# Performance work log

Hardware: AMD Instinct MI355X
Metric: run time of the kernel (lower is better)

The kernel has to match this reference:

```python
import jax, jax.numpy as jnp
import numpy as np

B, S, D, H = 2, 2048, 1024, 16
DK = D // H


def setup_inputs() -> dict:
    key = jax.random.key(0)
    ks = jax.random.split(key, 12)
    scale = 0.02  # keep exp(QK^T) finite in fp32
    return {
        "query": jax.random.normal(ks[0], (B, S, D), jnp.float32),
        "key_": jax.random.normal(ks[1], (B, S, D), jnp.float32),
        "value": jax.random.normal(ks[2], (B, S, D), jnp.float32),
        "mask": jax.random.randint(ks[3], (B, S, S), 0, 2, jnp.int32),
        "Wq": scale * jax.random.normal(ks[4], (D, D), jnp.float32),
        "bq": jnp.zeros((D,), jnp.float32),
        "Wk": scale * jax.random.normal(ks[5], (D, D), jnp.float32),
        "bk": jnp.zeros((D,), jnp.float32),
        "Wv": scale * jax.random.normal(ks[6], (D, D), jnp.float32),
        "bv": jnp.zeros((D,), jnp.float32),
        "Wo": scale * jax.random.normal(ks[7], (D, D), jnp.float32),
        "bo": jnp.zeros((D,), jnp.float32),
    }


def reference(query, key_, value, mask, Wq, bq, Wk, bk, Wv, bv, Wo, bo):
    b, s, d = query.shape
    # torch Linear: x @ W.T + b, then split heads -> [b, h, s, d_k]
    def proj(x, W, bias):
        return (x @ W.T + bias).reshape(b, s, H, DK).transpose(0, 2, 1, 3)

    q = proj(query, Wq, bq)
    k = proj(key_, Wk, bk)
    v = proj(value, Wv, bv)

    # non-standard: exp(QK^T) / sqrt(d_k), then mask, then softmax
    scores = jnp.exp(jnp.einsum("bhqd,bhkd->bhqk", q, k)) / jnp.sqrt(
        jnp.asarray(DK, q.dtype)
    )
    scores = jnp.where(mask[:, None, :, :] == 0, jnp.asarray(-1e9, q.dtype), scores)
    p_attn = jax.nn.softmax(scores, axis=-1)

    out = jnp.einsum("bhqk,bhkd->bhqd", p_attn, v)  # [b, h, s, d_k]
    out = out.transpose(0, 2, 1, 3).reshape(b, s, d)  # merge heads
    return out @ Wo.T + bo
```

## Files before the change

kernel.cpp:

```cpp
#include <hip/hip_runtime.h>
#include <math.h>

#define B_ 2
#define S_ 2048
#define D_ 1024
#define H_ 16
#define DK_ 64
#define M_ (B_*S_)

typedef __attribute__((ext_vector_type(8))) _Float16 f16x8;
typedef __attribute__((ext_vector_type(4))) _Float16 f16x4;
typedef __attribute__((ext_vector_type(2))) __fp16 fp16x2;
typedef __attribute__((ext_vector_type(4))) float f32x4;

#define MFMA16(a,b,c) __builtin_amdgcn_mfma_f32_16x16x32_f16((a),(b),(c),0,0,0)

__device__ __forceinline__ void gload16(const void* g, void* l) {
    __builtin_amdgcn_global_load_lds(
        (const __attribute__((address_space(1))) unsigned int*)g,
        (__attribute__((address_space(3))) unsigned int*)l, 16, 0, 0);
}

__global__ __launch_bounds__(256)
void splitmask(const float* __restrict__ query, const float* __restrict__ key_,
               const float* __restrict__ value,
               const float* __restrict__ Wq, const float* __restrict__ Wk,
               const float* __restrict__ Wv, const float* __restrict__ Wo,
               const int* __restrict__ mask, unsigned long long* __restrict__ mbits,
               _Float16* __restrict__ Xhq, _Float16* __restrict__ Xlq,
               _Float16* __restrict__ Xhk, _Float16* __restrict__ Xlk,
               _Float16* __restrict__ Xhv,
               _Float16* __restrict__ hq, _Float16* __restrict__ lq,
               _Float16* __restrict__ hk, _Float16* __restrict__ lk,
               _Float16* __restrict__ hv, _Float16* __restrict__ ho)
{
    if (blockIdx.x >= 8192) {
        int wid  = (blockIdx.x - 8192) * 4 + (threadIdx.x >> 6);
        int lane = threadIdx.x & 63;
        int v = mask[(size_t)wid * 64 + lane];
        unsigned long long bal = __ballot(v != 0);
        if (lane == 0) mbits[wid] = bal;
        return;
    }
    int t = blockIdx.x * 256 + threadIdx.x;
    int region = t >> 19;
    int u = t & 524287;
    const float* src; _Float16* dhi; _Float16* dlo; size_t e;
    if (region < 3) {
        e = (size_t)u * 8;
        src = (region == 0) ? query : (region == 1) ? key_ : value;
        dhi = (region == 0) ? Xhq : (region == 1) ? Xhk : Xhv;
        dlo = (region == 0) ? Xlq : (region == 1) ? Xlk : nullptr;
    } else {
        int mi = u >> 17;
        e = (size_t)(u & 131071) * 8;
        src = (mi == 0) ? Wq : (mi == 1) ? Wk : (mi == 2) ? Wv : Wo;
        dhi = (mi == 0) ? hq : (mi == 1) ? hk : (mi == 2) ? hv : ho;
        dlo = (mi == 0) ? lq : (mi == 1) ? lk : nullptr;
    }
    float4 a = *(const float4*)&src[e];
    float4 b = *(const float4*)&src[e + 4];
    float v[8] = {a.x, a.y, a.z, a.w, b.x, b.y, b.z, b.w};
    f16x8 hi, lo;
    #pragma unroll
    for (int j = 0; j < 8; ++j) {
        float s = v[j] * 64.f;
        _Float16 h = (_Float16)s;
        hi[j] = h; lo[j] = (_Float16)(s - (float)h);
    }
    *(f16x8*)&dhi[e] = hi;
    if (dlo) *(f16x8*)&dlo[e] = lo;
}

template<int NPROD, int OUT_MODE>
__device__ __forceinline__
void gemm_body2(char* smem, const _Float16* __restrict__ Ah,
                const _Float16* __restrict__ Al,
                const _Float16* __restrict__ Bh, const _Float16* __restrict__ Bl,
                const float* __restrict__ bias, void* __restrict__ outp, int gid)
{
    constexpr int BUFSZ = (NPROD == 3) ? 32768 : 16384;
    const int tid  = threadIdx.x;
    const int lane = tid & 63, w = tid >> 6;
    const int lx   = lane & 15, lg = lane >> 4;
    const int wm   = w >> 1, wn = w & 1;

    int nid = (gid & 7) * 32 + (gid >> 3);
    const int colBase = (nid & 7) * 128;
    const int rowBase = (nid >> 3) * 128;

    const int sRow = (lane >> 2);
    const int sChk = (lane & 3) ^ ((lane >> 2) & 3);

    auto STAGE = [&](int buf, int k0) {
        char* base = smem + buf * BUFSZ;
        #pragma unroll
        for (int ii = 0; ii < 2; ++ii) {
            int i = w * 2 + ii;
            int r = i * 16 + sRow;
            gload16(Ah + (size_t)(rowBase + r) * D_ + k0 + sChk * 8, base + i * 1024);
            gload16(Bh + (size_t)(colBase + r) * D_ + k0 + sChk * 8, base + 8192 + i * 1024);
            if (NPROD == 3) {
                gload16(Al + (size_t)(rowBase + r) * D_ + k0 + sChk * 8, base + 16384 + i * 1024);
                gload16(Bl + (size_t)(colBase + r) * D_ + k0 + sChk * 8, base + 24576 + i * 1024);
            }
        }
    };

    f32x4 acc[4][4];
    #pragma unroll
    for (int i = 0; i < 4; ++i)
        #pragma unroll
        for (int j = 0; j < 4; ++j) acc[i][j] = (f32x4){0.f, 0.f, 0.f, 0.f};

    STAGE(0, 0);
    __syncthreads();
    int cur = 0;
    for (int k0 = 0; k0 < D_; k0 += 32) {
        if (k0 + 32 < D_) STAGE(cur ^ 1, k0 + 32);
        char* base = smem + cur * BUFSZ;
        _Float16* AhS = (_Float16*)base;
        _Float16* BhS = (_Float16*)(base + 8192);
        _Float16* AlS = (_Float16*)(base + 16384);
        _Float16* BlS = (_Float16*)(base + 24576);

        f16x8 bh[4], bl[4];
        #pragma unroll
        for (int fj = 0; fj < 4; ++fj) {
            int brow = wn * 64 + fj * 16 + lx;
            bh[fj] = *(const f16x8*)((char*)BhS + brow * 64 + 16 * (lg ^ (brow & 3)));
            if (NPROD == 3)
                bl[fj] = *(const f16x8*)((char*)BlS + brow * 64 + 16 * (lg ^ (brow & 3)));
        }
        #pragma unroll
        for (int fi = 0; fi < 4; ++fi) {
            int arow = wm * 64 + fi * 16 + lx;
            f16x8 ah = *(const f16x8*)((char*)AhS + arow * 64 + 16 * (lg ^ (arow & 3)));
            f16x8 al;
            if (NPROD == 3)
                al = *(const f16x8*)((char*)AlS + arow * 64 + 16 * (lg ^ (arow & 3)));
            #pragma unroll
            for (int fj = 0; fj < 4; ++fj) {
                acc[fi][fj] = MFMA16(ah, bh[fj], acc[fi][fj]);
                if (NPROD == 3) {
                    acc[fi][fj] = MFMA16(ah, bl[fj], acc[fi][fj]);
                    acc[fi][fj] = MFMA16(al, bh[fj], acc[fi][fj]);
                }
            }
        }
        __syncthreads();
        cur ^= 1;
    }

    constexpr float INV = 1.f / 4096.f;
    #pragma unroll
    for (int fi = 0; fi < 4; ++fi) {
        #pragma unroll
        for (int fj = 0; fj < 4; ++fj) {
            int n = colBase + wn * 64 + fj * 16 + lx;
            float bv = bias[n];
            if (OUT_MODE == 1) {
                _Float16* Ohi = (_Float16*)outp;
                _Float16* Olo = Ohi + (size_t)M_ * D_;
                int hh = n >> 6, d = n & 63;
                #pragma unroll
                for (int rr = 0; rr < 4; ++rr) {
                    int m = rowBase + wm * 64 + fi * 16 + lg * 4 + rr;
                    int bb = m >> 11, s = m & 2047;
                    float val = acc[fi][fj][rr] * INV + bv;
                    _Float16 hv = (_Float16)val;
                    size_t o = (((size_t)bb * H_ + hh) * S_ + s) * DK_ + d;
                    Ohi[o] = hv;
                    Olo[o] = (_Float16)(val - (float)hv);
                }
            } else {
                _Float16* Vt = (_Float16*)outp;
                int hh = n >> 6, d = n & 63;
                int m0 = rowBase + wm * 64 + fi * 16 + lg * 4;
                int bb = m0 >> 11, s = m0 & 2047;
                f16x4 pk;
                #pragma unroll
                for (int rr = 0; rr < 4; ++rr)
                    pk[rr] = (_Float16)(acc[fi][fj][rr] * INV + bv);
                *(f16x4*)&Vt[(((size_t)bb * H_ + hh) * DK_ + d) * S_ + s] = pk;
            }
        }
    }
}

__global__ __launch_bounds__(256)
void proj3(const _Float16* __restrict__ Xhq, const _Float16* __restrict__ Xlq,
           const _Float16* __restrict__ Xhk, const _Float16* __restrict__ Xlk,
           const _Float16* __restrict__ Xhv,
           const _Float16* __restrict__ WhiQ, const _Float16* __restrict__ WloQ,
           const _Float16* __restrict__ WhiK, const _Float16* __restrict__ WloK,
           const _Float16* __restrict__ WhiV,
           const float* __restrict__ bq, const float* __restrict__ bk,
           const float* __restrict__ bv,
           _Float16* __restrict__ Qhi, _Float16* __restrict__ Khi,
           _Float16* __restrict__ VtW)
{
    extern __shared__ char smem[];
    int mode = blockIdx.x >> 8;
    int gid  = blockIdx.x & 255;
    if (mode == 0)
        gemm_body2<3, 1>(smem, Xhq, Xlq, WhiQ, WloQ, bq, Qhi, gid);
    else if (mode == 1)
        gemm_body2<3, 1>(smem, Xhk, Xlk, WhiK, WloK, bk, Khi, gid);
    else
        gemm_body2<1, 2>(smem, Xhv, nullptr, WhiV, nullptr, bv, VtW, gid);
}

__global__ __launch_bounds__(256)
void gemm64(const _Float16* __restrict__ Ap, const _Float16* __restrict__ Bhi,
            const float* __restrict__ bias, float* __restrict__ out)
{
    __shared__ __attribute__((aligned(16))) char smem[24576];

    const int tid  = threadIdx.x;
    const int lane = tid & 63, w = tid >> 6;
    const int lx   = lane & 15, lg = lane >> 4;
    const int wm   = w >> 1, wn = w & 1;

    int gid = blockIdx.x;
    int nid = (gid & 7) * 64 + (gid >> 3);
    const int colBase = (nid & 7) * 128;
    const int rowBase = (nid >> 3) * 64;

    const int sRow = (lane >> 2);
    const int sChk = (lane & 3) ^ ((lane >> 2) & 3);

    auto STAGE = [&](int buf, int k0) {
        char* base = smem + buf * 12288;
        gload16(Ap + (size_t)(rowBase + w * 16 + sRow) * D_ + k0 + sChk * 8,
                base + w * 1024);
        #pragma unroll
        for (int ii = 0; ii < 2; ++ii) {
            int i = w * 2 + ii;
            int r = i * 16 + sRow;
            gload16(Bhi + (size_t)(colBase + r) * D_ + k0 + sChk * 8,
                    base + 4096 + i * 1024);
        }
    };

    f32x4 acc[2][4];
    #pragma unroll
    for (int i = 0; i < 2; ++i)
        #pragma unroll
        for (int j = 0; j < 4; ++j) acc[i][j] = (f32x4){0.f, 0.f, 0.f, 0.f};

    STAGE(0, 0);
    __syncthreads();
    int cur = 0;
    for (int k0 = 0; k0 < D_; k0 += 32) {
        if (k0 + 32 < D_) STAGE(cur ^ 1, k0 + 32);
        char* base = smem + cur * 12288;
        _Float16* AS = (_Float16*)base;
        _Float16* BS = (_Float16*)(base + 4096);

        f16x8 bh[4];
        #pragma unroll
        for (int fj = 0; fj < 4; ++fj) {
            int brow = wn * 64 + fj * 16 + lx;
            bh[fj] = *(const f16x8*)((char*)BS + brow * 64 + 16 * (lg ^ (brow & 3)));
        }
        #pragma unroll
        for (int fi = 0; fi < 2; ++fi) {
            int arow = wm * 32 + fi * 16 + lx;
            f16x8 ah = *(const f16x8*)((char*)AS + arow * 64 + 16 * (lg ^ (arow & 3)));
            #pragma unroll
            for (int fj = 0; fj < 4; ++fj)
                acc[fi][fj] = MFMA16(ah, bh[fj], acc[fi][fj]);
        }
        __syncthreads();
        cur ^= 1;
    }

    constexpr float INV = 1.f / 64.f;
    #pragma unroll
    for (int fi = 0; fi < 2; ++fi) {
        #pragma unroll
        for (int fj = 0; fj < 4; ++fj) {
            int n = colBase + wn * 64 + fj * 16 + lx;
            float bv = bias[n];
            #pragma unroll
            for (int rr = 0; rr < 4; ++rr) {
                int m = rowBase + wm * 32 + fi * 16 + lg * 4 + rr;
                out[(size_t)m * D_ + n] = acc[fi][fj][rr] * INV + bv;
            }
        }
    }
}

__global__ __launch_bounds__(512, 4)
void flash_mfma(const _Float16* __restrict__ Qhi, const _Float16* __restrict__ Qlo,
                const _Float16* __restrict__ Khi, const _Float16* __restrict__ Klo,
                const _Float16* __restrict__ Vt, const unsigned long long* __restrict__ Mb,
                _Float16* __restrict__ octx)
{
    __shared__ __attribute__((aligned(16))) _Float16 Kbuf[2][2][64 * 64];
    __shared__ __attribute__((aligned(16))) _Float16 Vbuf[2][64 * 64];
    __shared__ __attribute__((aligned(16))) _Float16 PwS[8][16 * 64];

    const int tid  = threadIdx.x;
    const int lane = tid & 63;
    const int w    = tid >> 6;
    const int lx   = lane & 15;
    const int lg   = lane >> 4;

    int bid = blockIdx.x;
    int swz = (bid & 7) * 64 + (bid >> 3);
    int qb = swz & 15;
    int h  = (swz >> 4) & 15;
    int b  = swz >> 8;

    const int q0 = qb * 128;
    const size_t bh = (size_t)b * H_ + h;
    const _Float16* KhiG = Khi + bh * S_ * DK_;
    const _Float16* KloG = Klo + bh * S_ * DK_;
    const _Float16* VtG  = Vt  + bh * DK_ * S_;

    const int qrow = q0 + w * 16 + lx;
    f16x8 qh[2], ql[2];
    {
        const _Float16* ph = Qhi + bh * S_ * DK_ + (size_t)qrow * DK_ + lg * 8;
        const _Float16* pl = Qlo + bh * S_ * DK_ + (size_t)qrow * DK_ + lg * 8;
        qh[0] = *(const f16x8*)ph;
        qh[1] = *(const f16x8*)(ph + 32);
        ql[0] = *(const f16x8*)pl;
        ql[1] = *(const f16x8*)(pl + 32);
    }

    const unsigned long long* mrow = Mb + ((size_t)b * S_ + qrow) * (S_ / 64);
    constexpr float LN8 = 2.0794415416798357f;

    auto STAGE = [&](int buf, int t) {
        int rr = w * 8 + (lane >> 3);
        int cc = (lane & 7) ^ (lane >> 3);
        gload16(KhiG + (size_t)(t * 64 + rr) * DK_ + cc * 8, &Kbuf[buf][0][w * 512]);
        gload16(KloG + (size_t)(t * 64 + rr) * DK_ + cc * 8, &Kbuf[buf][1][w * 512]);
        gload16(VtG + (size_t)rr * S_ + t * 64 + cc * 8, &Vbuf[buf][w * 512]);
    };

    f32x4 oacc[4];
    float m_run = -1e30f, l_lane = 0.f;
    #pragma unroll
    for (int dt = 0; dt < 4; ++dt) oacc[dt] = (f32x4){0.f, 0.f, 0.f, 0.f};

    char* Pw = (char*)&PwS[w][0];

    STAGE(0, 0);
    int cur = 0;
    for (int t = 0; t < 32; ++t) {
        __syncthreads();
        if (t < 31) STAGE(cur ^ 1, t + 1);
        unsigned long long mw = mrow[t];
        const char* KH = (const char*)&Kbuf[cur][0][0];
        const char* KL = (const char*)&Kbuf[cur][1][0];
        const char* VB = (const char*)&Vbuf[cur][0];
        cur ^= 1;

        float sv[16];
        __builtin_amdgcn_s_setprio(1);
        #pragma unroll
        for (int ct = 0; ct < 4; ++ct) {
            int row  = ct * 16 + lx;
            int sw   = (row & 7) << 4;
            int base = row * 128 + lg * 16;
            f16x8 kh0 = *(const f16x8*)(KH + ((base +  0) ^ sw));
            f16x8 kh1 = *(const f16x8*)(KH + ((base + 64) ^ sw));
            f16x8 kl0 = *(const f16x8*)(KL + ((base +  0) ^ sw));
            f16x8 kl1 = *(const f16x8*)(KL + ((base + 64) ^ sw));
            f32x4 s = (f32x4){0.f, 0.f, 0.f, 0.f};
            s = MFMA16(kh0, qh[0], s);
            s = MFMA16(kh1, qh[1], s);
            s = MFMA16(kl0, qh[0], s);
            s = MFMA16(kl1, qh[1], s);
            s = MFMA16(kh0, ql[0], s);
            s = MFMA16(kh1, ql[1], s);
            #pragma unroll
            for (int r = 0; r < 4; ++r)
                sv[ct * 4 + r] = ((mw >> (lg * 4 + ct * 16 + r)) & 1ull)
                                   ? s[r] : -1e30f;
        }
        __builtin_amdgcn_s_setprio(0);

        float mx = fmaxf(fmaxf(fmaxf(sv[0], sv[1]), fmaxf(sv[2], sv[3])),
                         fmaxf(fmaxf(sv[4], sv[5]), fmaxf(sv[6], sv[7])));
        mx = fmaxf(mx, fmaxf(fmaxf(fmaxf(sv[8], sv[9]), fmaxf(sv[10], sv[11])),
                             fmaxf(fmaxf(sv[12], sv[13]), fmaxf(sv[14], sv[15]))));
        mx = fmaxf(mx, __shfl_xor(mx, 16));
        mx = fmaxf(mx, __shfl_xor(mx, 32));
        float tvmax = __expf(mx - LN8);

        if (__any(tvmax > m_run)) {
            float mn = fmaxf(m_run, tvmax);
            float scl = __expf(m_run - mn);
            m_run = mn;
            l_lane *= scl;
            #pragma unroll
            for (int dt = 0; dt < 4; ++dt)
                #pragma unroll
                for (int r = 0; r < 4; ++r) oacc[dt][r] *= scl;
        }

        float cut = (m_run >= 26.f) ? __logf(m_run - 25.f) + LN8 : -1e29f;
        if (__all(mx < cut)) continue;

        float mr = m_run;
        float pp[16];
        #pragma unroll
        for (int i = 0; i < 16; ++i) {
            float e = 0.f;
            if (__any(sv[i] > cut)) {
                float tv = __expf(sv[i] - LN8);
                e = __expf(tv - mr);
                e = (sv[i] > cut) ? e : 0.f;
                l_lane += e;
            }
            pp[i] = e;
        }

        {
            int psw = (lx & 7) << 4;
            #pragma unroll
            for (int ct = 0; ct < 4; ++ct) {
                fp16x2 a = __builtin_amdgcn_cvt_pkrtz(pp[ct * 4 + 0], pp[ct * 4 + 1]);
                fp16x2 c = __builtin_amdgcn_cvt_pkrtz(pp[ct * 4 + 2], pp[ct * 4 + 3]);
                unsigned int au, cu;
                __builtin_memcpy(&au, &a, 4);
                __builtin_memcpy(&cu, &c, 4);
                int off = lx * 128 + ct * 32 + lg * 8;
                *(unsigned int*)(Pw + ((off + 0) ^ psw)) = au;
                *(unsigned int*)(Pw + ((off + 4) ^ psw)) = cu;
            }
        }

        f16x8 pa0, pa1;
        {
            int psw = (lx & 7) << 4;
            int pb  = lx * 128 + lg * 16;
            pa0 = *(const f16x8*)(Pw + ((pb +  0) ^ psw));
            pa1 = *(const f16x8*)(Pw + ((pb + 64) ^ psw));
        }
        __builtin_amdgcn_s_setprio(1);
        #pragma unroll
        for (int dt = 0; dt < 4; ++dt) {
            int vrow = dt * 16 + lx;
            int vs   = (vrow & 7) << 4;
            int vb   = vrow * 128 + lg * 16;
            f16x8 v0 = *(const f16x8*)(VB + ((vb +  0) ^ vs));
            f16x8 v1 = *(const f16x8*)(VB + ((vb + 64) ^ vs));
            oacc[dt] = MFMA16(v0, pa0, oacc[dt]);
            oacc[dt] = MFMA16(v1, pa1, oacc[dt]);
        }
        __builtin_amdgcn_s_setprio(0);
    }

    float l = l_lane;
    l += __shfl_xor(l, 16);
    l += __shfl_xor(l, 32);
    {
        float inv = 1.0f / l;
        #pragma unroll
        for (int dt = 0; dt < 4; ++dt) {
            f16x4 o;
            #pragma unroll
            for (int r = 0; r < 4; ++r) o[r] = (_Float16)(oacc[dt][r] * inv);
            *(f16x4*)&octx[((size_t)b * S_ + qrow) * D_ + h * DK_ + dt * 16 + lg * 4] = o;
        }
    }
}

extern "C" void kernel_launch(void* const* d_in, const int* in_sizes, int n_in,
                              void* d_out, int out_size, void* d_ws, size_t ws_size,
                              hipStream_t stream)
{
    const float* query = (const float*)d_in[0];
    const float* key_  = (const float*)d_in[1];
    const float* value = (const float*)d_in[2];
    const int*   mask  = (const int*)d_in[3];
    const float* Wq = (const float*)d_in[4];
    const float* bq = (const float*)d_in[5];
    const float* Wk = (const float*)d_in[6];
    const float* bk = (const float*)d_in[7];
    const float* Wv = (const float*)d_in[8];
    const float* bv = (const float*)d_in[9];
    const float* Wo = (const float*)d_in[10];
    const float* bo = (const float*)d_in[11];

    char* p = (char*)d_ws;
    unsigned long long* mbits = (unsigned long long*)p;  p += (size_t)1 << 20;
    _Float16* WhiQ = (_Float16*)p;  p += (size_t)2 << 20;
    _Float16* WloQ = (_Float16*)p;  p += (size_t)2 << 20;
    _Float16* WhiK = (_Float16*)p;  p += (size_t)2 << 20;
    _Float16* WloK = (_Float16*)p;  p += (size_t)2 << 20;
    _Float16* WhiV = (_Float16*)p;  p += (size_t)2 << 20;
    _Float16* WhiO = (_Float16*)p;  p += (size_t)2 << 20;
    _Float16* Xhq  = (_Float16*)p;  p += (size_t)8 << 20;
    _Float16* Xlq  = (_Float16*)p;  p += (size_t)8 << 20;
    _Float16* Xhk  = (_Float16*)p;  p += (size_t)8 << 20;
    _Float16* Xlk  = (_Float16*)p;  p += (size_t)8 << 20;
    _Float16* Xhv  = (_Float16*)p;  p += (size_t)8 << 20;
    _Float16* Qhi  = (_Float16*)p;  p += (size_t)16 << 20;
    _Float16* Khi  = (_Float16*)p;  p += (size_t)16 << 20;
    _Float16* VtW  = (_Float16*)p;  p += (size_t)8 << 20;
    _Float16* octx = (_Float16*)p;  p += (size_t)8 << 20;
    float* out = (float*)d_out;

    _Float16* Qlo = Qhi + (size_t)M_ * D_;
    _Float16* Klo = Khi + (size_t)M_ * D_;

    splitmask<<<8192 + 32768, 256, 0, stream>>>(query, key_, value,
                                                Wq, Wk, Wv, Wo, mask, mbits,
                                                Xhq, Xlq, Xhk, Xlk, Xhv,
                                                WhiQ, WloQ, WhiK, WloK, WhiV, WhiO);

    proj3<<<768, 256, 65536, stream>>>(Xhq, Xlq, Xhk, Xlk, Xhv,
                                       WhiQ, WloQ, WhiK, WloK, WhiV,
                                       bq, bk, bv, Qhi, Khi, VtW);

    flash_mfma<<<512, 512, 0, stream>>>(Qhi, Qlo, Khi, Klo, VtW, mbits, octx);

    gemm64<<<512, 256, 0, stream>>>(octx, WhiO, bo, out);
}
```

Before: 197.2 us.

## Fuse activation fp16 split into projection GEMM and unroll flash tile loop

The projection GEMM now reads fp32 query/key/value directly. It splits each value into hi/lo fp16 parts in registers and writes them into the swizzled LDS tile, so the separate split pass and its 40MB of intermediate fp16 buffers are gone. The A operand moves from async global-to-LDS loads to register-staged loads, with the conversion placed after the MFMA loop to overlap latency. The flash attention loop is unrolled by two with fixed double-buffer indices, and mask bit extraction is simplified to 32-bit shifts. The risk is extra VALU work and register pressure in the GEMM main loop.

```diff
diff --git a/kernel.cpp b/kernel.cpp
--- a/kernel.cpp
+++ b/kernel.cpp
@@ -22,20 +22,15 @@
 }
 
 __global__ __launch_bounds__(256)
-void splitmask(const float* __restrict__ query, const float* __restrict__ key_,
-               const float* __restrict__ value,
-               const float* __restrict__ Wq, const float* __restrict__ Wk,
+void splitmask(const float* __restrict__ Wq, const float* __restrict__ Wk,
                const float* __restrict__ Wv, const float* __restrict__ Wo,
                const int* __restrict__ mask, unsigned long long* __restrict__ mbits,
-               _Float16* __restrict__ Xhq, _Float16* __restrict__ Xlq,
-               _Float16* __restrict__ Xhk, _Float16* __restrict__ Xlk,
-               _Float16* __restrict__ Xhv,
                _Float16* __restrict__ hq, _Float16* __restrict__ lq,
                _Float16* __restrict__ hk, _Float16* __restrict__ lk,
                _Float16* __restrict__ hv, _Float16* __restrict__ ho)
 {
-    if (blockIdx.x >= 8192) {
-        int wid  = (blockIdx.x - 8192) * 4 + (threadIdx.x >> 6);
+    if (blockIdx.x >= 2048) {
+        int wid  = (blockIdx.x - 2048) * 4 + (threadIdx.x >> 6);
         int lane = threadIdx.x & 63;
         int v = mask[(size_t)wid * 64 + lane];
         unsigned long long bal = __ballot(v != 0);
@@ -43,21 +38,11 @@
         return;
     }
     int t = blockIdx.x * 256 + threadIdx.x;
-    int region = t >> 19;
-    int u = t & 524287;
-    const float* src; _Float16* dhi; _Float16* dlo; size_t e;
-    if (region < 3) {
-        e = (size_t)u * 8;
-        src = (region == 0) ? query : (region == 1) ? key_ : value;
-        dhi = (region == 0) ? Xhq : (region == 1) ? Xhk : Xhv;
-        dlo = (region == 0) ? Xlq : (region == 1) ? Xlk : nullptr;
-    } else {
-        int mi = u >> 17;
-        e = (size_t)(u & 131071) * 8;
-        src = (mi == 0) ? Wq : (mi == 1) ? Wk : (mi == 2) ? Wv : Wo;
-        dhi = (mi == 0) ? hq : (mi == 1) ? hk : (mi == 2) ? hv : ho;
-        dlo = (mi == 0) ? lq : (mi == 1) ? lk : nullptr;
-    }
+    int mi = t >> 17;
+    size_t e = (size_t)(t & 131071) * 8;
+    const float* src = (mi == 0) ? Wq : (mi == 1) ? Wk : (mi == 2) ? Wv : Wo;
+    _Float16* dhi = (mi == 0) ? hq : (mi == 1) ? hk : (mi == 2) ? hv : ho;
+    _Float16* dlo = (mi == 0) ? lq : (mi == 1) ? lk : nullptr;
     float4 a = *(const float4*)&src[e];
     float4 b = *(const float4*)&src[e + 4];
     float v[8] = {a.x, a.y, a.z, a.w, b.x, b.y, b.z, b.w};
@@ -74,8 +59,7 @@
 
 template<int NPROD, int OUT_MODE>
 __device__ __forceinline__
-void gemm_body2(char* smem, const _Float16* __restrict__ Ah,
-                const _Float16* __restrict__ Al,
+void gemm_body3(char* smem, const float* __restrict__ Xf,
                 const _Float16* __restrict__ Bh, const _Float16* __restrict__ Bl,
                 const float* __restrict__ bias, void* __restrict__ outp, int gid)
 {
@@ -91,19 +75,45 @@
 
     const int sRow = (lane >> 2);
     const int sChk = (lane & 3) ^ ((lane >> 2) & 3);
-
-    auto STAGE = [&](int buf, int k0) {
+    const int sr = tid >> 1, sh = tid & 1;
+
+    auto STAGE_B = [&](int buf, int k0) {
         char* base = smem + buf * BUFSZ;
         #pragma unroll
         for (int ii = 0; ii < 2; ++ii) {
             int i = w * 2 + ii;
             int r = i * 16 + sRow;
-            gload16(Ah + (size_t)(rowBase + r) * D_ + k0 + sChk * 8, base + i * 1024);
             gload16(Bh + (size_t)(colBase + r) * D_ + k0 + sChk * 8, base + 8192 + i * 1024);
-            if (NPROD == 3) {
-                gload16(Al + (size_t)(rowBase + r) * D_ + k0 + sChk * 8, base + 16384 + i * 1024);
+            if (NPROD == 3)
                 gload16(Bl + (size_t)(colBase + r) * D_ + k0 + sChk * 8, base + 24576 + i * 1024);
-            }
+        }
+    };
+    auto LOAD_A = [&](int k0, float4* xr) {
+        const float* ap = Xf + (size_t)(rowBase + sr) * D_ + k0 + sh * 16;
+        xr[0] = *(const float4*)ap;
+        xr[1] = *(const float4*)(ap + 4);
+        xr[2] = *(const float4*)(ap + 8);
+        xr[3] = *(const float4*)(ap + 12);
+    };
+    auto WRITE_A = [&](int buf, const float4* xr) {
+        float xv[16] = {xr[0].x,xr[0].y,xr[0].z,xr[0].w, xr[1].x,xr[1].y,xr[1].z,xr[1].w,
+                        xr[2].x,xr[2].y,xr[2].z,xr[2].w, xr[3].x,xr[3].y,xr[3].z,xr[3].w};
+        f16x8 hi[2], lo[2];
+        #pragma unroll
+        for (int j = 0; j < 16; ++j) {
+            float s = xv[j] * 64.f;
+            _Float16 hv = (_Float16)s;
+            hi[j >> 3][j & 7] = hv;
+            if (NPROD == 3) lo[j >> 3][j & 7] = (_Float16)(s - (float)hv);
+        }
+        char* bp = smem + buf * BUFSZ + sr * 64;
+        int c0 = sh * 2;
+        *(f16x8*)(bp + 16 * ((c0 + 0) ^ (sr & 3))) = hi[0];
+        *(f16x8*)(bp + 16 * ((c0 + 1) ^ (sr & 3))) = hi[1];
+        if (NPROD == 3) {
+            char* lp = bp + 16384;
+            *(f16x8*)(lp + 16 * ((c0 + 0) ^ (sr & 3))) = lo[0];
+            *(f16x8*)(lp + 16 * ((c0 + 1) ^ (sr & 3))) = lo[1];
         }
     };
 
@@ -113,11 +123,18 @@
         #pragma unroll
         for (int j = 0; j < 4; ++j) acc[i][j] = (f32x4){0.f, 0.f, 0.f, 0.f};
 
-    STAGE(0, 0);
+    float4 xr[4];
+    STAGE_B(0, 0);
+    LOAD_A(0, xr);
+    WRITE_A(0, xr);
     __syncthreads();
     int cur = 0;
     for (int k0 = 0; k0 < D_; k0 += 32) {
-        if (k0 + 32 < D_) STAGE(cur ^ 1, k0 + 32);
+        const bool more = (k0 + 32 < D_);
+        if (more) {
+            LOAD_A(k0 + 32, xr);
+            STAGE_B(cur ^ 1, k0 + 32);
+        }
         char* base = smem + cur * BUFSZ;
         _Float16* AhS = (_Float16*)base;
         _Float16* BhS = (_Float16*)(base + 8192);
@@ -148,6 +165,7 @@
                 }
             }
         }
+        if (more) WRITE_A(cur ^ 1, xr);
         __syncthreads();
         cur ^= 1;
     }
@@ -189,9 +207,8 @@
 }
 
 __global__ __launch_bounds__(256)
-void proj3(const _Float16* __restrict__ Xhq, const _Float16* __restrict__ Xlq,
-           const _Float16* __restrict__ Xhk, const _Float16* __restrict__ Xlk,
-           const _Float16* __restrict__ Xhv,
+void proj3(const float* __restrict__ query, const float* __restrict__ key_,
+           const float* __restrict__ value,
            const _Float16* __restrict__ WhiQ, const _Float16* __restrict__ WloQ,
            const _Float16* __restrict__ WhiK, const _Float16* __restrict__ WloK,
            const _Float16* __restrict__ WhiV,
@@ -204,11 +221,11 @@
     int mode = blockIdx.x >> 8;
     int gid  = blockIdx.x & 255;
     if (mode == 0)
-        gemm_body2<3, 1>(smem, Xhq, Xlq, WhiQ, WloQ, bq, Qhi, gid);
+        gemm_body3<3, 1>(smem, query, WhiQ, WloQ, bq, Qhi, gid);
     else if (mode == 1)
-        gemm_body2<3, 1>(smem, Xhk, Xlk, WhiK, WloK, bk, Khi, gid);
+        gemm_body3<3, 1>(smem, key_, WhiK, WloK, bk, Khi, gid);
     else
-        gemm_body2<1, 2>(smem, Xhv, nullptr, WhiV, nullptr, bv, VtW, gid);
+        gemm_body3<1, 2>(smem, value, WhiV, nullptr, bv, VtW, gid);
 }
 
 __global__ __launch_bounds__(256)
@@ -349,16 +366,10 @@
 
     char* Pw = (char*)&PwS[w][0];
 
-    STAGE(0, 0);
-    int cur = 0;
-    for (int t = 0; t < 32; ++t) {
-        __syncthreads();
-        if (t < 31) STAGE(cur ^ 1, t + 1);
+    auto TILE = [&](int t, const char* KH, const char* KL, const char* VB) {
         unsigned long long mw = mrow[t];
-        const char* KH = (const char*)&Kbuf[cur][0][0];
-        const char* KL = (const char*)&Kbuf[cur][1][0];
-        const char* VB = (const char*)&Vbuf[cur][0];
-        cur ^= 1;
+        unsigned mlo = (unsigned)(mw >> (lg * 4));
+        unsigned mhi = (unsigned)(mw >> 32) >> (lg * 4);
 
         float sv[16];
         __builtin_amdgcn_s_setprio(1);
@@ -378,10 +389,11 @@
             s = MFMA16(kl1, qh[1], s);
             s = MFMA16(kh0, ql[0], s);
             s = MFMA16(kh1, ql[1], s);
+            unsigned mm = (ct < 2) ? mlo : mhi;
+            int sh0 = (ct & 1) * 16;
             #pragma unroll
             for (int r = 0; r < 4; ++r)
-                sv[ct * 4 + r] = ((mw >> (lg * 4 + ct * 16 + r)) & 1ull)
-                                   ? s[r] : -1e30f;
+                sv[ct * 4 + r] = ((mm >> (sh0 + r)) & 1u) ? s[r] : -1e30f;
         }
         __builtin_amdgcn_s_setprio(0);
 
@@ -405,7 +417,7 @@
         }
 
         float cut = (m_run >= 26.f) ? __logf(m_run - 25.f) + LN8 : -1e29f;
-        if (__all(mx < cut)) continue;
+        if (__all(mx < cut)) return;
 
         float mr = m_run;
         float pp[16];
@@ -455,6 +467,19 @@
             oacc[dt] = MFMA16(v1, pa1, oacc[dt]);
         }
         __builtin_amdgcn_s_setprio(0);
+    };
+
+    STAGE(0, 0);
+    #pragma unroll 1
+    for (int t = 0; t < 32; t += 2) {
+        __syncthreads();
+        STAGE(1, t + 1);
+        TILE(t, (const char*)&Kbuf[0][0][0], (const char*)&Kbuf[0][1][0],
+             (const char*)&Vbuf[0][0]);
+        __syncthreads();
+        if (t + 2 < 32) STAGE(0, t + 2);
+        TILE(t + 1, (const char*)&Kbuf[1][0][0], (const char*)&Kbuf[1][1][0],
+             (const char*)&Vbuf[1][0]);
     }
 
     float l = l_lane;
@@ -497,11 +522,6 @@
     _Float16* WloK = (_Float16*)p;  p += (size_t)2 << 20;
     _Float16* WhiV = (_Float16*)p;  p += (size_t)2 << 20;
     _Float16* WhiO = (_Float16*)p;  p += (size_t)2 << 20;
-    _Float16* Xhq  = (_Float16*)p;  p += (size_t)8 << 20;
-    _Float16* Xlq  = (_Float16*)p;  p += (size_t)8 << 20;
-    _Float16* Xhk  = (_Float16*)p;  p += (size_t)8 << 20;
-    _Float16* Xlk  = (_Float16*)p;  p += (size_t)8 << 20;
-    _Float16* Xhv  = (_Float16*)p;  p += (size_t)8 << 20;
     _Float16* Qhi  = (_Float16*)p;  p += (size_t)16 << 20;
     _Float16* Khi  = (_Float16*)p;  p += (size_t)16 << 20;
     _Float16* VtW  = (_Float16*)p;  p += (size_t)8 << 20;
@@ -511,12 +531,10 @@
     _Float16* Qlo = Qhi + (size_t)M_ * D_;
     _Float16* Klo = Khi + (size_t)M_ * D_;
 
-    splitmask<<<8192 + 32768, 256, 0, stream>>>(query, key_, value,
-                                                Wq, Wk, Wv, Wo, mask, mbits,
-                                                Xhq, Xlq, Xhk, Xlk, Xhv,
+    splitmask<<<2048 + 32768, 256, 0, stream>>>(Wq, Wk, Wv, Wo, mask, mbits,
                                                 WhiQ, WloQ, WhiK, WloK, WhiV, WhiO);
 
-    proj3<<<768, 256, 65536, stream>>>(Xhq, Xlq, Xhk, Xlk, Xhv,
+    proj3<<<768, 256, 65536, stream>>>(query, key_, value,
                                        WhiQ, WloQ, WhiK, WloK, WhiV,
                                        bq, bk, bv, Qhi, Khi, VtW);
 
```

Measured after the change: 197.5 us. No clear change (+0.1%).
